# Optimization experiments

Measured on AMD Instinct MI355X. Metric: run time of the kernel, lower is better.

## Reference

```python
import jax, jax.numpy as jnp
import numpy as np

B, N, D, S, H = 64, 4096, 256, 8, 256
ITERS = 3
EPS = 1e-8
SCALE = D ** -0.5


def _ln(x, g, b):
    m = jnp.mean(x, axis=-1, keepdims=True)
    v = jnp.mean((x - m) ** 2, axis=-1, keepdims=True)
    return (x - m) * jax.lax.rsqrt(v + 1e-5) * g + b


def setup_inputs() -> dict:
    key = jax.random.key(0)
    ks = jax.random.split(key, 12)
    s = 0.02
    return {
        'inputs': jax.random.normal(ks[0], (B, N, D), jnp.float32),
        'slot_noise': jax.random.normal(ks[1], (B, S, D), jnp.float32),
        'slots_mean': jax.random.normal(ks[2], (1, 1, D), jnp.float32),
        'slots_logvar': s * jax.random.normal(ks[3], (1, 1, D), jnp.float32),
        'Wq': s * jax.random.normal(ks[4], (D, D), jnp.float32),
        'bq': jnp.zeros((D,), jnp.float32),
        'Wk': s * jax.random.normal(ks[5], (D, D), jnp.float32),
        'bk': jnp.zeros((D,), jnp.float32),
        'Wv': s * jax.random.normal(ks[6], (D, D), jnp.float32),
        'bv': jnp.zeros((D,), jnp.float32),
        'W_ih': s * jax.random.normal(ks[7], (3 * D, D), jnp.float32),
        'b_ih': jnp.zeros((3 * D,), jnp.float32),
        'W_hh': s * jax.random.normal(ks[8], (3 * D, D), jnp.float32),
        'b_hh': jnp.zeros((3 * D,), jnp.float32),
        'W1': s * jax.random.normal(ks[9], (H, D), jnp.float32),
        'b1': jnp.zeros((H,), jnp.float32),
        'W2': s * jax.random.normal(ks[10], (D, H), jnp.float32),
        'b2': jnp.zeros((D,), jnp.float32),
        'g_in': jnp.ones((D,), jnp.float32),
        'bias_in': jnp.zeros((D,), jnp.float32),
        'g_slots': jnp.ones((D,), jnp.float32),
        'bias_slots': jnp.zeros((D,), jnp.float32),
        'g_ff': jnp.ones((D,), jnp.float32),
        'bias_ff': jnp.zeros((D,), jnp.float32),
    }


def reference(inputs, slot_noise, slots_mean, slots_logvar, Wq, bq, Wk, bk, Wv, bv,
              W_ih, b_ih, W_hh, b_hh, W1, b1, W2, b2,
              g_in, bias_in, g_slots, bias_slots, g_ff, bias_ff):
    # slot init: mean + exp(logvar) * noise  (exp(logvar) used as multiplier, as in source)
    slots = slots_mean + jnp.exp(slots_logvar) * slot_noise  # [B,S,D]
    x = _ln(inputs, g_in, bias_in)                            # [B,N,D]
    k = x @ Wk.T + bk
    v = x @ Wv.T + bv
    attn = None
    for _ in range(ITERS):
        slots_prev = slots
        sn = _ln(slots, g_slots, bias_slots)
        q = sn @ Wq.T + bq                                    # [B,S,D]
        dots = jnp.einsum('bid,bjd->bij', q, k) * SCALE       # [B,S,N]
        attn = jax.nn.softmax(dots, axis=1) + EPS             # softmax over slots, no renorm
        updates = jnp.einsum('bjd,bij->bid', v, attn)         # [B,S,D]
        # GRUCell (PyTorch convention)
        gi = updates @ W_ih.T + b_ih                          # [B,S,3D]
        gh = slots_prev @ W_hh.T + b_hh
        i_r, i_z, i_n = jnp.split(gi, 3, axis=-1)
        h_r, h_z, h_n = jnp.split(gh, 3, axis=-1)
        r = jax.nn.sigmoid(i_r + h_r)
        z = jax.nn.sigmoid(i_z + h_z)
        n = jnp.tanh(i_n + r * h_n)
        slots = (1.0 - z) * n + z * slots_prev
        # MLP residual
        sf = _ln(slots, g_ff, bias_ff)
        slots = slots + (jax.nn.relu(sf @ W1.T + b1) @ W2.T + b2)
    return (slots, attn)
```

## Files before the change

### kernel.cpp

```cpp
#include <hip/hip_runtime.h>

typedef unsigned short u16;
typedef __bf16 bf16x8 __attribute__((ext_vector_type(8)));
typedef float f32x4 __attribute__((ext_vector_type(4)));

#define DEV static __device__ __forceinline__

DEV u16 f2bf(float f) {
    unsigned int u = __builtin_bit_cast(unsigned int, f);
    u += 0x7FFFu + ((u >> 16) & 1u);
    return (u16)(u >> 16);
}

DEV bf16x8 frag_ld(const u16* p) {
    return __builtin_bit_cast(bf16x8, *(const uint4*)p);
}

DEV float sigm(float x) { return 1.f / (1.f + __expf(-x)); }

DEV int swz(int idx, int d) { return idx ^ (((d >> 3) & 3) << 4); }

__global__ void kInit(const float* __restrict__ noise, const float* __restrict__ mean,
                      const float* __restrict__ logv, float* __restrict__ slots) {
    int id = blockIdx.x * 256 + threadIdx.x;
    int d = id & 255;
    slots[id] = mean[d] + __expf(logv[d]) * noise[id];
}

__global__ void kT(const float* __restrict__ in, float* __restrict__ out, int R, int C) {
    __shared__ float tile[32][33];
    const int tx = threadIdx.x & 31, ty = threadIdx.x >> 5;
    const int c0 = blockIdx.x * 32, r0 = blockIdx.y * 32;
    #pragma unroll
    for (int i = 0; i < 4; ++i)
        tile[ty + i * 8][tx] = in[(size_t)(r0 + ty + i * 8) * C + c0 + tx];
    __syncthreads();
    #pragma unroll
    for (int i = 0; i < 4; ++i)
        out[(size_t)(c0 + ty + i * 8) * R + r0 + tx] = tile[tx][ty + i * 8];
}

__global__ void kWqk(const float* __restrict__ Wq, const float* __restrict__ Wk,
                     const float* __restrict__ bq, const float* __restrict__ bk,
                     float* __restrict__ Wqk, float* __restrict__ wbc) {
    const int a = blockIdx.x, e = threadIdx.x;
    if (a < 256) {
        float acc = 0.f;
        for (int d = 0; d < 256; ++d) acc += Wq[(size_t)d * 256 + a] * Wk[(size_t)d * 256 + e];
        Wqk[(size_t)a * 256 + e] = acc;
    } else if (a == 256) {
        float acc = 0.f;
        for (int d = 0; d < 256; ++d) acc += bq[d] * Wk[(size_t)d * 256 + e];
        wbc[e] = acc;
    } else {
        float acc = 0.f;
        for (int d = 0; d < 256; ++d) acc += Wq[(size_t)d * 256 + e] * bk[d];
        wbc[256 + e] = acc;
        if (e == 0) {
            float c0 = 0.f;
            for (int d = 0; d < 256; ++d) c0 += bq[d] * bk[d];
            wbc[512] = c0;
        }
    }
}

__global__ __launch_bounds__(256) void kLN(
    const float* __restrict__ X, const float* __restrict__ g, const float* __restrict__ bb,
    u16* __restrict__ XN)
{
    const int w = threadIdx.x >> 6, lane = threadIdx.x & 63;
    const int c = lane << 2;
    const float4 g4 = *(const float4*)(g + c);
    const float4 b4 = *(const float4*)(bb + c);
    const size_t r0 = (size_t)blockIdx.x * 128 + (size_t)w * 32;
    #pragma unroll 4
    for (int i = 0; i < 32; ++i) {
        const float4 x = *(const float4*)(X + (r0 + i) * 256 + c);
        float s1 = x.x + x.y + x.z + x.w;
        float s2 = x.x * x.x + x.y * x.y + x.z * x.z + x.w * x.w;
        #pragma unroll
        for (int o = 32; o > 0; o >>= 1) { s1 += __shfl_xor(s1, o); s2 += __shfl_xor(s2, o); }
        const float mu = s1 * (1.f / 256.f);
        const float rs = rsqrtf(s2 * (1.f / 256.f) - mu * mu + 1e-5f);
        ushort4 pk;
        pk.x = f2bf((x.x - mu) * rs * g4.x + b4.x);
        pk.y = f2bf((x.y - mu) * rs * g4.y + b4.y);
        pk.z = f2bf((x.z - mu) * rs * g4.z + b4.z);
        pk.w = f2bf((x.w - mu) * rs * g4.w + b4.w);
        *(ushort4*)(XN + (r0 + i) * 256 + c) = pk;
    }
}

__global__ __launch_bounds__(256) void kSn(
    const float* __restrict__ slots, const float* __restrict__ gs, const float* __restrict__ bs,
    const float* __restrict__ Wqk, const float* __restrict__ wbc,
    u16* __restrict__ qo, float* __restrict__ qc)
{
    __shared__ float SN[8][256];
    __shared__ float red2[4][8][64];
    const int t = threadIdx.x;
    const int b = blockIdx.y, seg = blockIdx.x;
    const int w = t >> 6, lane = t & 63;
    #pragma unroll
    for (int rr = 0; rr < 2; ++rr) {
        const int r = w * 2 + rr;
        const int c = lane * 4;
        const float4 x = *(const float4*)(slots + ((size_t)b * 8 + r) * 256 + c);
        float s1 = x.x + x.y + x.z + x.w;
        float s2 = x.x * x.x + x.y * x.y + x.z * x.z + x.w * x.w;
        #pragma unroll
        for (int o = 32; o > 0; o >>= 1) { s1 += __shfl_xor(s1, o); s2 += __shfl_xor(s2, o); }
        const float mu = s1 * (1.f / 256.f);
        const float rs = rsqrtf(s2 * (1.f / 256.f) - mu * mu + 1e-5f);
        const float4 g4 = *(const float4*)(gs + c);
        const float4 b4 = *(const float4*)(bs + c);
        SN[r][c + 0] = (x.x - mu) * rs * g4.x + b4.x;
        SN[r][c + 1] = (x.y - mu) * rs * g4.y + b4.y;
        SN[r][c + 2] = (x.z - mu) * rs * g4.z + b4.z;
        SN[r][c + 3] = (x.w - mu) * rs * g4.w + b4.w;
    }
    __syncthreads();
    const int c = seg * 64 + (t & 63);
    const int p = t >> 6;
    float acc[8] = {};
    #pragma unroll 4
    for (int d = p * 64; d < p * 64 + 64; ++d) {
        const float wq = Wqk[(size_t)d * 256 + c];
        #pragma unroll
        for (int r = 0; r < 8; ++r) acc[r] += wq * SN[r][d];
    }
    #pragma unroll
    for (int r = 0; r < 8; ++r) red2[p][r][t & 63] = acc[r];
    __syncthreads();
    const float bb = wbc[c];
    #pragma unroll
    for (int rr = t >> 6; rr < 8; rr += 4) {
        const float s = red2[0][rr][t & 63] + red2[1][rr][t & 63]
                      + red2[2][rr][t & 63] + red2[3][rr][t & 63];
        qo[((size_t)b * 16 + rr) * 256 + c] = f2bf((s + bb) * 0.0625f);
    }
    if (seg == 0) {
        const int r = t >> 5, l = t & 31;
        float a = 0.f;
        #pragma unroll
        for (int d8 = 0; d8 < 8; ++d8) a += SN[r][l * 8 + d8] * wbc[256 + l * 8 + d8];
        #pragma unroll
        for (int o = 16; o > 0; o >>= 1) a += __shfl_xor(a, o);
        if (l == 0) qc[(size_t)b * 8 + r] = 0.0625f * (a + wbc[512]);
    }
}

__global__ __launch_bounds__(256, 2) void kF(
    const u16* __restrict__ Q,
    const float* __restrict__ qcg,
    const u16* __restrict__ XN,
    float* __restrict__ attn_out,
    float* __restrict__ part,
    float* __restrict__ part2,
    int write_attn)
{
    __shared__ __align__(16) u16 T2[256 * 136];
    __shared__ __align__(16) u16 att[16 * 136];
    __shared__ float sred[4][2][4][16];
    const int tid = threadIdx.x;
    const int w = tid >> 6, lane = tid & 63;
    const int quad = lane >> 4, l16 = lane & 15;
    const int b = blockIdx.y, nt = blockIdx.x;
    const int j0 = nt << 9;

    const u16* qb = Q + (size_t)b * 16 * 256;
    bf16x8 qfrag[8];
    #pragma unroll
    for (int k0 = 0; k0 < 8; ++k0)
        qfrag[k0] = frag_ld(qb + l16 * 256 + k0 * 32 + quad * 8);

    float c8[8];
    #pragma unroll
    for (int i = 0; i < 8; ++i) c8[i] = qcg[(size_t)b * 8 + i];

    for (int idx = tid; idx < 8 * 136; idx += 256) att[8 * 136 + idx] = 0;

    f32x4 us[4] = {};
    float sacc[4] = {};

    const u16* xb = XN + ((size_t)b * 4096 + j0) * 256;
    const int qb1 = (quad & 1) << 2;

    for (int st = 0; st < 4; ++st) {
        __syncthreads();
        f32x4 dacc[2] = {};
        #pragma unroll
        for (int n2 = 0; n2 < 2; ++n2) {
            const int jsl = w * 32 + n2 * 16 + l16;
            const u16* xrow = xb + ((size_t)(st * 128 + jsl)) * 256;
            #pragma unroll
            for (int k0 = 0; k0 < 8; ++k0) {
                const uint4 raw = *(const uint4*)(xrow + k0 * 32 + quad * 8);
                dacc[n2] = __builtin_amdgcn_mfma_f32_16x16x32_bf16(
                    qfrag[k0], __builtin_bit_cast(bf16x8, raw), dacc[n2], 0, 0, 0);
                const u16* h = (const u16*)&raw;
                const int dbase = k0 * 32 + quad * 8;
                #pragma unroll
                for (int e = 0; e < 8; ++e)
                    T2[swz((dbase + e) * 136 + jsl, dbase + e)] = h[e];
            }
        }
        #pragma unroll
        for (int n2 = 0; n2 < 2; ++n2) {
            const int jsl = w * 32 + n2 * 16 + l16;
            float v[8];
            #pragma unroll
            for (int r = 0; r < 4; ++r) {
                v[qb1 + r]       = dacc[n2][r];
                v[(qb1 ^ 4) + r] = __shfl_xor(dacc[n2][r], 16);
            }
            #pragma unroll
            for (int i = 0; i < 8; ++i) v[i] += c8[i];
            float m = v[0];
            #pragma unroll
            for (int i = 1; i < 8; ++i) m = fmaxf(m, v[i]);
            float s = 0.f;
            #pragma unroll
            for (int i = 0; i < 8; ++i) { v[i] = __expf(v[i] - m); s += v[i]; }
            const float inv = 1.f / s;
            if (quad < 2) {
                #pragma unroll
                for (int r = 0; r < 4; ++r) {
                    const float a = v[qb1 + r] * inv + 1e-8f;
                    att[(qb1 + r) * 136 + jsl] = f2bf(a);
                    sacc[r] += a;
                    if (write_attn)
                        attn_out[((size_t)b * 8 + qb1 + r) * 4096 + j0 + st * 128 + jsl] = a;
                }
            }
        }
        __syncthreads();
        bf16x8 afrag[4];
        #pragma unroll
        for (int k0 = 0; k0 < 4; ++k0)
            afrag[k0] = frag_ld(att + l16 * 136 + k0 * 32 + quad * 8);
        #pragma unroll
        for (int n2 = 0; n2 < 4; ++n2) {
            const int d = w * 64 + n2 * 16 + l16;
            #pragma unroll
            for (int k0 = 0; k0 < 4; ++k0) {
                const bf16x8 bfr = frag_ld(T2 + swz(d * 136 + k0 * 32 + quad * 8, d));
                us[n2] = __builtin_amdgcn_mfma_f32_16x16x32_bf16(afrag[k0], bfr, us[n2], 0, 0, 0);
            }
        }
    }

    if (quad < 2) {
        #pragma unroll
        for (int r = 0; r < 4; ++r) sred[w][quad][r][l16] = sacc[r];
        #pragma unroll
        for (int n2 = 0; n2 < 4; ++n2)
            #pragma unroll
            for (int r = 0; r < 4; ++r)
                part[(((size_t)nt * 64 + b) * 8 + (quad * 4 + r)) * 256 + w * 64 + n2 * 16 + l16]
                    = us[n2][r];
    }
    __syncthreads();
    if (tid < 8) {
        const int q = tid >> 2, r = tid & 3;
        float s = 0.f;
        #pragma unroll
        for (int ww = 0; ww < 4; ++ww)
            #pragma unroll
            for (int l = 0; l < 16; ++l) s += sred[ww][q][r][l];
        part2[((size_t)nt * 64 + b) * 8 + tid] = s;
    }
}

__global__ __launch_bounds__(256) void kB3(
    const float* __restrict__ part, const float* __restrict__ part2,
    const float* __restrict__ WvT, const float* __restrict__ bv,
    const float* __restrict__ sl_in,
    const float* __restrict__ WihT, const float* __restrict__ bih,
    const float* __restrict__ WhhT, const float* __restrict__ bhh,
    const float* __restrict__ W1T, const float* __restrict__ b1,
    const float* __restrict__ W2T, const float* __restrict__ b2,
    const float* __restrict__ gf, const float* __restrict__ bff,
    float* __restrict__ sl_out)
{
    __shared__ float Ul[2][256], Sl[2][256];
    __shared__ float red[2][4][6][256];
    __shared__ float SNl[2][256];
    __shared__ float cw[2][2][4];
    __shared__ float Ssl[2];
    const int t = threadIdx.x;
    const int kp = t >> 6, c = t & 63;
    const int row0 = blockIdx.x * 2;

    #pragma unroll
    for (int r = 0; r < 2; ++r) {
        const int row = row0 + r;
        const int b = row >> 3, s = row & 7;
        float u = 0.f;
        #pragma unroll
        for (int nt = 0; nt < 8; ++nt)
            u += part[(((size_t)nt * 64 + b) * 8 + s) * 256 + t];
        Ul[r][t] = u;
        Sl[r][t] = sl_in[(size_t)row * 256 + t];
    }
    if (t < 2) {
        const int row = row0 + t;
        const int b = row >> 3, s = row & 7;
        float ss = 0.f;
        #pragma unroll
        for (int nt = 0; nt < 8; ++nt) ss += part2[((size_t)nt * 64 + b) * 8 + s];
        Ssl[t] = ss;
    }
    __syncthreads();

    {
        float va[2][4] = {};
        #pragma unroll 4
        for (int dd = 0; dd < 64; ++dd) {
            const int d = kp * 64 + dd;
            const float* wr = WvT + (size_t)d * 256;
            const float u0 = Ul[0][d], u1 = Ul[1][d];
            #pragma unroll
            for (int cg = 0; cg < 4; ++cg) {
                const float wv = wr[cg * 64 + c];
                va[0][cg] += wv * u0;
                va[1][cg] += wv * u1;
            }
        }
        #pragma unroll
        for (int r = 0; r < 2; ++r)
            #pragma unroll
            for (int cg = 0; cg < 4; ++cg)
                red[r][kp][0][cg * 64 + c] = va[r][cg];
    }
    __syncthreads();
    const float bvt = bv[t];
    float upd2[2];
    #pragma unroll
    for (int r = 0; r < 2; ++r)
        upd2[r] = red[r][0][0][t] + red[r][1][0][t] + red[r][2][0][t] + red[r][3][0][t]
                + Ssl[r] * bvt;
    __syncthreads();
    #pragma unroll
    for (int r = 0; r < 2; ++r) Ul[r][t] = upd2[r];
    __syncthreads();

    float ga[2][4][6] = {};
    #pragma unroll 2
    for (int dd = 0; dd < 64; ++dd) {
        const int d = kp * 64 + dd;
        const float* wi = WihT + (size_t)d * 768;
        const float* wh = WhhT + (size_t)d * 768;
        const float u0 = Ul[0][d], u1 = Ul[1][d];
        const float s0 = Sl[0][d], s1 = Sl[1][d];
        #pragma unroll
        for (int cg = 0; cg < 4; ++cg) {
            const int t2 = cg * 64 + c;
            const float wa = wi[t2], wb = wi[256 + t2], wc = wi[512 + t2];
            const float wd = wh[t2], we = wh[256 + t2], wf = wh[512 + t2];
            ga[0][cg][0] += wa * u0; ga[0][cg][1] += wb * u0; ga[0][cg][2] += wc * u0;
            ga[0][cg][3] += wd * s0; ga[0][cg][4] += we * s0; ga[0][cg][5] += wf * s0;
            ga[1][cg][0] += wa * u1; ga[1][cg][1] += wb * u1; ga[1][cg][2] += wc * u1;
            ga[1][cg][3] += wd * s1; ga[1][cg][4] += we * s1; ga[1][cg][5] += wf * s1;
        }
    }
    #pragma unroll
    for (int r = 0; r < 2; ++r)
        #pragma unroll
        for (int cg = 0; cg < 4; ++cg)
            #pragma unroll
            for (int g = 0; g < 6; ++g)
                red[r][kp][g][cg * 64 + c] = ga[r][cg][g];
    __syncthreads();

    const float b_ir = bih[t], b_iz = bih[256 + t], b_in = bih[512 + t];
    const float b_hr = bhh[t], b_hz = bhh[256 + t], b_hn = bhh[512 + t];
    float hnew[2];
    #pragma unroll
    for (int r = 0; r < 2; ++r) {
        float s6[6];
        #pragma unroll
        for (int g = 0; g < 6; ++g)
            s6[g] = red[r][0][g][t] + red[r][1][g][t] + red[r][2][g][t] + red[r][3][g][t];
        const float rg = sigm(s6[0] + b_ir + s6[3] + b_hr);
        const float zg = sigm(s6[1] + b_iz + s6[4] + b_hz);
        const float ng = tanhf(s6[2] + b_in + rg * (s6[5] + b_hn));
        hnew[r] = (1.f - zg) * ng + zg * Sl[r][t];
    }
    #pragma unroll
    for (int r = 0; r < 2; ++r) {
        float s1 = hnew[r], s2 = hnew[r] * hnew[r];
        #pragma unroll
        for (int o = 32; o > 0; o >>= 1) { s1 += __shfl_xor(s1, o); s2 += __shfl_xor(s2, o); }
        if (c == 0) { cw[r][0][kp] = s1; cw[r][1][kp] = s2; }
    }
    __syncthreads();
    const float gft = gf[t], bfft = bff[t];
    #pragma unroll
    for (int r = 0; r < 2; ++r) {
        const float s1 = cw[r][0][0] + cw[r][0][1] + cw[r][0][2] + cw[r][0][3];
        const float s2 = cw[r][1][0] + cw[r][1][1] + cw[r][1][2] + cw[r][1][3];
        const float mu = s1 * (1.f / 256.f);
        const float rs = rsqrtf(s2 * (1.f / 256.f) - mu * mu + 1e-5f);
        SNl[r][t] = (hnew[r] - mu) * rs * gft + bfft;
    }
    __syncthreads();

    {
        float m1[2][4] = {};
        #pragma unroll 4
        for (int dd = 0; dd < 64; ++dd) {
            const int d = kp * 64 + dd;
            const float* wr = W1T + (size_t)d * 256;
            const float n0 = SNl[0][d], n1 = SNl[1][d];
            #pragma unroll
            for (int cg = 0; cg < 4; ++cg) {
                const float wv = wr[cg * 64 + c];
                m1[0][cg] += wv * n0;
                m1[1][cg] += wv * n1;
            }
        }
        #pragma unroll
        for (int r = 0; r < 2; ++r)
            #pragma unroll
            for (int cg = 0; cg < 4; ++cg)
                red[r][kp][0][cg * 64 + c] = m1[r][cg];
    }
    __syncthreads();
    const float b1t = b1[t];
    float h1v[2];
    #pragma unroll
    for (int r = 0; r < 2; ++r)
        h1v[r] = fmaxf(red[r][0][0][t] + red[r][1][0][t] + red[r][2][0][t] + red[r][3][0][t]
                       + b1t, 0.f);
    __syncthreads();
    #pragma unroll
    for (int r = 0; r < 2; ++r) SNl[r][t] = h1v[r];
    __syncthreads();
    {
        float m2[2][4] = {};
        #pragma unroll 4
        for (int dd = 0; dd < 64; ++dd) {
            const int d = kp * 64 + dd;
            const float* wr = W2T + (size_t)d * 256;
            const float x0 = SNl[0][d], x1 = SNl[1][d];
            #pragma unroll
            for (int cg = 0; cg < 4; ++cg) {
                const float wv = wr[cg * 64 + c];
                m2[0][cg] += wv * x0;
                m2[1][cg] += wv * x1;
            }
        }
        #pragma unroll
        for (int r = 0; r < 2; ++r)
            #pragma unroll
            for (int cg = 0; cg < 4; ++cg)
                red[r][kp][1][cg * 64 + c] = m2[r][cg];
    }
    __syncthreads();
    const float b2t = b2[t];
    #pragma unroll
    for (int r = 0; r < 2; ++r) {
        const float o = red[r][0][1][t] + red[r][1][1][t] + red[r][2][1][t] + red[r][3][1][t];
        sl_out[(size_t)(row0 + r) * 256 + t] = hnew[r] + o + b2t;
    }
}

extern "C" void kernel_launch(void* const* d_in, const int* in_sizes, int n_in,
                              void* d_out, int out_size, void* d_ws, size_t ws_size,
                              hipStream_t stream) {
    const float* inputs = (const float*)d_in[0];
    const float* noise  = (const float*)d_in[1];
    const float* smean  = (const float*)d_in[2];
    const float* slogv  = (const float*)d_in[3];
    const float* Wq  = (const float*)d_in[4];
    const float* bq  = (const float*)d_in[5];
    const float* Wk  = (const float*)d_in[6];
    const float* bk  = (const float*)d_in[7];
    const float* Wv  = (const float*)d_in[8];
    const float* bv  = (const float*)d_in[9];
    const float* Wih = (const float*)d_in[10];
    const float* bih = (const float*)d_in[11];
    const float* Whh = (const float*)d_in[12];
    const float* bhh = (const float*)d_in[13];
    const float* W1  = (const float*)d_in[14];
    const float* b1  = (const float*)d_in[15];
    const float* W2  = (const float*)d_in[16];
    const float* b2  = (const float*)d_in[17];
    const float* gin = (const float*)d_in[18];
    const float* bin = (const float*)d_in[19];
    const float* gs  = (const float*)d_in[20];
    const float* bs  = (const float*)d_in[21];
    const float* gf  = (const float*)d_in[22];
    const float* bff = (const float*)d_in[23];

    char* ws = (char*)d_ws;
    u16*  XNw    = (u16*)(ws);
    u16*  qw     = (u16*)(ws + 134217728ull);
    float* slots = (float*)(ws + 134742016ull);
    float* Wqkw  = (float*)(ws + 135790592ull);
    float* wbc   = (float*)(ws + 136052736ull);
    float* qcw   = (float*)(ws + 136056832ull);
    float* WvT   = (float*)(ws + 136060928ull);
    float* WihT  = (float*)(ws + 136323072ull);
    float* WhhT  = (float*)(ws + 137109504ull);
    float* W1T   = (float*)(ws + 137895936ull);
    float* W2T   = (float*)(ws + 138158080ull);
    float* partw = (float*)(ws + 138420224ull);
    float* part2w= (float*)(ws + 142614528ull);

    float* out = (float*)d_out;
    float* attn_out = out + 131072;

    kInit<<<512, 256, 0, stream>>>(noise, smean, slogv, slots);
    kWqk<<<258, 256, 0, stream>>>(Wq, Wk, bq, bk, Wqkw, wbc);
    kT<<<dim3(8, 8),  256, 0, stream>>>(Wv,  WvT,  256, 256);
    kT<<<dim3(8, 24), 256, 0, stream>>>(Wih, WihT, 768, 256);
    kT<<<dim3(8, 24), 256, 0, stream>>>(Whh, WhhT, 768, 256);
    kT<<<dim3(8, 8),  256, 0, stream>>>(W1,  W1T,  256, 256);
    kT<<<dim3(8, 8),  256, 0, stream>>>(W2,  W2T,  256, 256);
    kLN<<<2048, 256, 0, stream>>>(inputs, gin, bin, XNw);
    for (int it = 0; it < 3; ++it) {
        kSn<<<dim3(4, 64), 256, 0, stream>>>(slots, gs, bs, Wqkw, wbc, qw, qcw);
        kF<<<dim3(8, 64), 256, 0, stream>>>(qw, qcw, XNw, attn_out, partw, part2w, it == 2);
        kB3<<<256, 256, 0, stream>>>(partw, part2w, WvT, bv, slots,
                                     WihT, bih, WhhT, bhh, W1T, b1, W2T, b2, gf, bff,
                                     (it == 2) ? out : slots);
    }
}
```

Measured before the change: 718.3 us.

## Replace LDS-transposed MFMA attn@X with per-wave FP32 FMA accumulation

The second product (attention times normalized inputs) no longer transposes X into shared memory and runs it through MFMA. Each wave instead re-reads its own X rows from global/L2 and accumulates all 8 slots × 8 dims per lane in FP32 registers with FMAs. Partial sums are combined across half-waves by shuffle and across waves through shared memory before the write-out. This drops the heavy scattered 16-bit LDS stores and two barriers per step. In exchange it re-reads X, does the math on scalar FMA units instead of matrix cores, and keeps 64 accumulators per lane, which raises register pressure.

```diff
diff --git a/kernel.cpp b/kernel.cpp
--- a/kernel.cpp
+++ b/kernel.cpp
@@ -18,7 +18,8 @@
 
 DEV float sigm(float x) { return 1.f / (1.f + __expf(-x)); }
 
-DEV int swz(int idx, int d) { return idx ^ (((d >> 3) & 3) << 4); }
+DEV float blo(unsigned u) { return __builtin_bit_cast(float, u << 16); }
+DEV float bhi(unsigned u) { return __builtin_bit_cast(float, u & 0xffff0000u); }
 
 __global__ void kInit(const float* __restrict__ noise, const float* __restrict__ mean,
                       const float* __restrict__ logv, float* __restrict__ slots) {
@@ -159,12 +160,13 @@
     float* __restrict__ part2,
     int write_attn)
 {
-    __shared__ __align__(16) u16 T2[256 * 136];
-    __shared__ __align__(16) u16 att[16 * 136];
+    __shared__ __align__(16) float att32[128][8];
+    __shared__ float usred[4][8][256];
     __shared__ float sred[4][2][4][16];
     const int tid = threadIdx.x;
     const int w = tid >> 6, lane = tid & 63;
     const int quad = lane >> 4, l16 = lane & 15;
+    const int dsg = lane & 31, jg = lane >> 5;
     const int b = blockIdx.y, nt = blockIdx.x;
     const int j0 = nt << 9;
 
@@ -178,16 +180,17 @@
     #pragma unroll
     for (int i = 0; i < 8; ++i) c8[i] = qcg[(size_t)b * 8 + i];
 
-    for (int idx = tid; idx < 8 * 136; idx += 256) att[8 * 136 + idx] = 0;
-
-    f32x4 us[4] = {};
+    float acc[8][8];
+    #pragma unroll
+    for (int i = 0; i < 8; ++i)
+        #pragma unroll
+        for (int e = 0; e < 8; ++e) acc[i][e] = 0.f;
     float sacc[4] = {};
 
     const u16* xb = XN + ((size_t)b * 4096 + j0) * 256;
     const int qb1 = (quad & 1) << 2;
 
     for (int st = 0; st < 4; ++st) {
-        __syncthreads();
         f32x4 dacc[2] = {};
         #pragma unroll
         for (int n2 = 0; n2 < 2; ++n2) {
@@ -195,14 +198,9 @@
             const u16* xrow = xb + ((size_t)(st * 128 + jsl)) * 256;
             #pragma unroll
             for (int k0 = 0; k0 < 8; ++k0) {
-                const uint4 raw = *(const uint4*)(xrow + k0 * 32 + quad * 8);
+                const bf16x8 bfr = frag_ld(xrow + k0 * 32 + quad * 8);
                 dacc[n2] = __builtin_amdgcn_mfma_f32_16x16x32_bf16(
-                    qfrag[k0], __builtin_bit_cast(bf16x8, raw), dacc[n2], 0, 0, 0);
-                const u16* h = (const u16*)&raw;
-                const int dbase = k0 * 32 + quad * 8;
-                #pragma unroll
-                for (int e = 0; e < 8; ++e)
-                    T2[swz((dbase + e) * 136 + jsl, dbase + e)] = h[e];
+                    qfrag[k0], bfr, dacc[n2], 0, 0, 0);
             }
         }
         #pragma unroll
@@ -224,43 +222,71 @@
             for (int i = 0; i < 8; ++i) { v[i] = __expf(v[i] - m); s += v[i]; }
             const float inv = 1.f / s;
             if (quad < 2) {
-                #pragma unroll
-                for (int r = 0; r < 4; ++r) {
-                    const float a = v[qb1 + r] * inv + 1e-8f;
-                    att[(qb1 + r) * 136 + jsl] = f2bf(a);
-                    sacc[r] += a;
-                    if (write_attn)
-                        attn_out[((size_t)b * 8 + qb1 + r) * 4096 + j0 + st * 128 + jsl] = a;
+                float4 av;
+                av.x = v[qb1 + 0] * inv + 1e-8f;
+                av.y = v[qb1 + 1] * inv + 1e-8f;
+                av.z = v[qb1 + 2] * inv + 1e-8f;
+                av.w = v[qb1 + 3] * inv + 1e-8f;
+                sacc[0] += av.x; sacc[1] += av.y; sacc[2] += av.z; sacc[3] += av.w;
+                *(float4*)&att32[jsl][qb1] = av;
+                if (write_attn) {
+                    attn_out[((size_t)b * 8 + qb1 + 0) * 4096 + j0 + st * 128 + jsl] = av.x;
+                    attn_out[((size_t)b * 8 + qb1 + 1) * 4096 + j0 + st * 128 + jsl] = av.y;
+                    attn_out[((size_t)b * 8 + qb1 + 2) * 4096 + j0 + st * 128 + jsl] = av.z;
+                    attn_out[((size_t)b * 8 + qb1 + 3) * 4096 + j0 + st * 128 + jsl] = av.w;
                 }
             }
         }
-        __syncthreads();
-        bf16x8 afrag[4];
-        #pragma unroll
-        for (int k0 = 0; k0 < 4; ++k0)
-            afrag[k0] = frag_ld(att + l16 * 136 + k0 * 32 + quad * 8);
-        #pragma unroll
-        for (int n2 = 0; n2 < 4; ++n2) {
-            const int d = w * 64 + n2 * 16 + l16;
-            #pragma unroll
-            for (int k0 = 0; k0 < 4; ++k0) {
-                const bf16x8 bfr = frag_ld(T2 + swz(d * 136 + k0 * 32 + quad * 8, d));
-                us[n2] = __builtin_amdgcn_mfma_f32_16x16x32_bf16(afrag[k0], bfr, us[n2], 0, 0, 0);
-            }
-        }
-    }
-
+        #pragma unroll 4
+        for (int jj = 0; jj < 16; ++jj) {
+            const int jsl = w * 32 + jj * 2 + jg;
+            const uint4 raw = *(const uint4*)(xb + ((size_t)(st * 128 + jsl)) * 256 + dsg * 8);
+            const float4 a0 = *(const float4*)&att32[jsl][0];
+            const float4 a1 = *(const float4*)&att32[jsl][4];
+            float xf[8];
+            xf[0] = blo(raw.x); xf[1] = bhi(raw.x);
+            xf[2] = blo(raw.y); xf[3] = bhi(raw.y);
+            xf[4] = blo(raw.z); xf[5] = bhi(raw.z);
+            xf[6] = blo(raw.w); xf[7] = bhi(raw.w);
+            #pragma unroll
+            for (int e = 0; e < 8; ++e) {
+                acc[0][e] = fmaf(a0.x, xf[e], acc[0][e]);
+                acc[1][e] = fmaf(a0.y, xf[e], acc[1][e]);
+                acc[2][e] = fmaf(a0.z, xf[e], acc[2][e]);
+                acc[3][e] = fmaf(a0.w, xf[e], acc[3][e]);
+                acc[4][e] = fmaf(a1.x, xf[e], acc[4][e]);
+                acc[5][e] = fmaf(a1.y, xf[e], acc[5][e]);
+                acc[6][e] = fmaf(a1.z, xf[e], acc[6][e]);
+                acc[7][e] = fmaf(a1.w, xf[e], acc[7][e]);
+            }
+        }
+    }
+
+    #pragma unroll
+    for (int i = 0; i < 8; ++i)
+        #pragma unroll
+        for (int e = 0; e < 8; ++e) acc[i][e] += __shfl_xor(acc[i][e], 32);
+    if (jg == 0) {
+        #pragma unroll
+        for (int i = 0; i < 8; ++i) {
+            float4 lo, hi;
+            lo.x = acc[i][0]; lo.y = acc[i][1]; lo.z = acc[i][2]; lo.w = acc[i][3];
+            hi.x = acc[i][4]; hi.y = acc[i][5]; hi.z = acc[i][6]; hi.w = acc[i][7];
+            *(float4*)&usred[w][i][dsg * 8]     = lo;
+            *(float4*)&usred[w][i][dsg * 8 + 4] = hi;
+        }
+    }
     if (quad < 2) {
         #pragma unroll
         for (int r = 0; r < 4; ++r) sred[w][quad][r][l16] = sacc[r];
-        #pragma unroll
-        for (int n2 = 0; n2 < 4; ++n2)
-            #pragma unroll
-            for (int r = 0; r < 4; ++r)
-                part[(((size_t)nt * 64 + b) * 8 + (quad * 4 + r)) * 256 + w * 64 + n2 * 16 + l16]
-                    = us[n2][r];
-    }
-    __syncthreads();
+    }
+    __syncthreads();
+    #pragma unroll
+    for (int i = 0; i < 8; ++i) {
+        const float s = usred[0][i][tid] + usred[1][i][tid]
+                      + usred[2][i][tid] + usred[3][i][tid];
+        part[(((size_t)nt * 64 + b) * 8 + i) * 256 + tid] = s;
+    }
     if (tid < 8) {
         const int q = tid >> 2, r = tid & 3;
         float s = 0.f;
```

After: 733.5 us. 2.1% more time.

## Split fused attention kernel into dots/softmax and update kernels with pre-transposed XN

Applied to the files above, without the earlier changes.

Replaces the fused kF kernel, which transposed the normalized inputs through a large LDS tile every iteration, with a one-time bf16 transpose of XN into a feature-major copy plus two kernels. kD computes dots and the softmax and writes bf16 attention to global memory, and kU computes the updates by MFMA against the transposed XN. Both use finer 128-token tiles, so there are 32 partials instead of 8, and kB3 now sums more partials. It also merges the setup kernels into one launch. The aim is to drop the heavy LDS scatter and raise occupancy, at the cost of an extra 128MB transpose and additional global traffic each iteration.

```diff
diff --git a/kernel.cpp b/kernel.cpp
--- a/kernel.cpp
+++ b/kernel.cpp
@@ -18,50 +18,65 @@
 
 DEV float sigm(float x) { return 1.f / (1.f + __expf(-x)); }
 
-DEV int swz(int idx, int d) { return idx ^ (((d >> 3) & 3) << 4); }
-
-__global__ void kInit(const float* __restrict__ noise, const float* __restrict__ mean,
-                      const float* __restrict__ logv, float* __restrict__ slots) {
-    int id = blockIdx.x * 256 + threadIdx.x;
-    int d = id & 255;
-    slots[id] = mean[d] + __expf(logv[d]) * noise[id];
-}
-
-__global__ void kT(const float* __restrict__ in, float* __restrict__ out, int R, int C) {
+__global__ __launch_bounds__(256) void kSetup(
+    const float* __restrict__ noise, const float* __restrict__ mean,
+    const float* __restrict__ logv, float* __restrict__ slots,
+    const float* __restrict__ Wq, const float* __restrict__ Wk,
+    const float* __restrict__ bq, const float* __restrict__ bk,
+    float* __restrict__ Wqk, float* __restrict__ wbc,
+    const float* __restrict__ Wv,  float* __restrict__ WvT,
+    const float* __restrict__ Wih, float* __restrict__ WihT,
+    const float* __restrict__ Whh, float* __restrict__ WhhT,
+    const float* __restrict__ W1,  float* __restrict__ W1T,
+    const float* __restrict__ W2,  float* __restrict__ W2T)
+{
     __shared__ float tile[32][33];
-    const int tx = threadIdx.x & 31, ty = threadIdx.x >> 5;
-    const int c0 = blockIdx.x * 32, r0 = blockIdx.y * 32;
+    const int bid = blockIdx.x, t = threadIdx.x;
+    if (bid < 512) {
+        const int id = bid * 256 + t;
+        const int d = id & 255;
+        slots[id] = mean[d] + __expf(logv[d]) * noise[id];
+        return;
+    }
+    if (bid < 770) {
+        const int a = bid - 512, e = t;
+        if (a < 256) {
+            float acc = 0.f;
+            for (int d = 0; d < 256; ++d) acc += Wq[(size_t)d * 256 + a] * Wk[(size_t)d * 256 + e];
+            Wqk[(size_t)a * 256 + e] = acc;
+        } else if (a == 256) {
+            float acc = 0.f;
+            for (int d = 0; d < 256; ++d) acc += bq[d] * Wk[(size_t)d * 256 + e];
+            wbc[e] = acc;
+        } else {
+            float acc = 0.f;
+            for (int d = 0; d < 256; ++d) acc += Wq[(size_t)d * 256 + e] * bk[d];
+            wbc[256 + e] = acc;
+            if (e == 0) {
+                float c0 = 0.f;
+                for (int d = 0; d < 256; ++d) c0 += bq[d] * bk[d];
+                wbc[512] = c0;
+            }
+        }
+        return;
+    }
+    const int rb = bid - 770;
+    const float* in; float* outp; int R, k;
+    if (rb < 64)       { in = Wv;  outp = WvT;  R = 256; k = rb; }
+    else if (rb < 256) { in = Wih; outp = WihT; R = 768; k = rb - 64; }
+    else if (rb < 448) { in = Whh; outp = WhhT; R = 768; k = rb - 256; }
+    else if (rb < 512) { in = W1;  outp = W1T;  R = 256; k = rb - 448; }
+    else               { in = W2;  outp = W2T;  R = 256; k = rb - 512; }
+    const int bx = k & 7, by = k >> 3;
+    const int tx = t & 31, ty = t >> 5;
+    const int c0 = bx * 32, r0 = by * 32;
     #pragma unroll
     for (int i = 0; i < 4; ++i)
-        tile[ty + i * 8][tx] = in[(size_t)(r0 + ty + i * 8) * C + c0 + tx];
+        tile[ty + i * 8][tx] = in[(size_t)(r0 + ty + i * 8) * 256 + c0 + tx];
     __syncthreads();
     #pragma unroll
     for (int i = 0; i < 4; ++i)
-        out[(size_t)(c0 + ty + i * 8) * R + r0 + tx] = tile[tx][ty + i * 8];
-}
-
-__global__ void kWqk(const float* __restrict__ Wq, const float* __restrict__ Wk,
-                     const float* __restrict__ bq, const float* __restrict__ bk,
-                     float* __restrict__ Wqk, float* __restrict__ wbc) {
-    const int a = blockIdx.x, e = threadIdx.x;
-    if (a < 256) {
-        float acc = 0.f;
-        for (int d = 0; d < 256; ++d) acc += Wq[(size_t)d * 256 + a] * Wk[(size_t)d * 256 + e];
-        Wqk[(size_t)a * 256 + e] = acc;
-    } else if (a == 256) {
-        float acc = 0.f;
-        for (int d = 0; d < 256; ++d) acc += bq[d] * Wk[(size_t)d * 256 + e];
-        wbc[e] = acc;
-    } else {
-        float acc = 0.f;
-        for (int d = 0; d < 256; ++d) acc += Wq[(size_t)d * 256 + e] * bk[d];
-        wbc[256 + e] = acc;
-        if (e == 0) {
-            float c0 = 0.f;
-            for (int d = 0; d < 256; ++d) c0 += bq[d] * bk[d];
-            wbc[512] = c0;
-        }
-    }
+        outp[(size_t)(c0 + ty + i * 8) * R + r0 + tx] = tile[tx][ty + i * 8];
 }
 
 __global__ __launch_bounds__(256) void kLN(
@@ -91,6 +106,34 @@
     }
 }
 
+__global__ __launch_bounds__(256) void kT16(
+    const u16* __restrict__ XN, u16* __restrict__ XNT)
+{
+    __shared__ ushort2 S[64][33];
+    const int t = threadIdx.x;
+    const int jt = blockIdx.x, dt = blockIdx.y, b = blockIdx.z;
+    const int j0 = jt << 6, d0 = dt << 6;
+    const u16* in = XN + (size_t)b * 4096 * 256;
+    u16* outp = XNT + (size_t)b * 256 * 4096;
+    const int tx = t & 31, ty = t >> 5;
+    #pragma unroll
+    for (int i = 0; i < 8; ++i) {
+        const int j = ty + i * 8;
+        S[j][tx] = *(const ushort2*)(in + (size_t)(j0 + j) * 256 + d0 + tx * 2);
+    }
+    __syncthreads();
+    const int tx2 = t & 31, ty2 = t >> 5;
+    #pragma unroll
+    for (int i = 0; i < 8; ++i) {
+        const int d = ty2 + i * 8;
+        const ushort2 a = S[tx2 * 2 + 0][d >> 1];
+        const ushort2 bq2 = S[tx2 * 2 + 1][d >> 1];
+        ushort2 v;
+        if (ty2 & 1) { v.x = a.y; v.y = bq2.y; } else { v.x = a.x; v.y = bq2.x; }
+        *(ushort2*)(outp + (size_t)(d0 + d) * 4096 + j0 + tx2 * 2) = v;
+    }
+}
+
 __global__ __launch_bounds__(256) void kSn(
     const float* __restrict__ slots, const float* __restrict__ gs, const float* __restrict__ bs,
     const float* __restrict__ Wqk, const float* __restrict__ wbc,
@@ -150,125 +193,127 @@
     }
 }
 
-__global__ __launch_bounds__(256, 2) void kF(
+__global__ __launch_bounds__(256) void kD(
     const u16* __restrict__ Q,
     const float* __restrict__ qcg,
     const u16* __restrict__ XN,
+    u16* __restrict__ att,
     float* __restrict__ attn_out,
-    float* __restrict__ part,
     float* __restrict__ part2,
     int write_attn)
 {
-    __shared__ __align__(16) u16 T2[256 * 136];
-    __shared__ __align__(16) u16 att[16 * 136];
-    __shared__ float sred[4][2][4][16];
+    __shared__ float sred[4][2][4];
     const int tid = threadIdx.x;
     const int w = tid >> 6, lane = tid & 63;
     const int quad = lane >> 4, l16 = lane & 15;
-    const int b = blockIdx.y, nt = blockIdx.x;
-    const int j0 = nt << 9;
-
-    const u16* qb = Q + (size_t)b * 16 * 256;
+    const int qb1 = (quad & 1) << 2;
+    const int b = blockIdx.y, js = blockIdx.x;
+    const int j0 = js << 7;
+
+    const u16* qptr = Q + (size_t)b * 16 * 256;
     bf16x8 qfrag[8];
     #pragma unroll
     for (int k0 = 0; k0 < 8; ++k0)
-        qfrag[k0] = frag_ld(qb + l16 * 256 + k0 * 32 + quad * 8);
+        qfrag[k0] = frag_ld(qptr + l16 * 256 + k0 * 32 + quad * 8);
 
     float c8[8];
     #pragma unroll
     for (int i = 0; i < 8; ++i) c8[i] = qcg[(size_t)b * 8 + i];
 
-    for (int idx = tid; idx < 8 * 136; idx += 256) att[8 * 136 + idx] = 0;
-
-    f32x4 us[4] = {};
     float sacc[4] = {};
-
     const u16* xb = XN + ((size_t)b * 4096 + j0) * 256;
-    const int qb1 = (quad & 1) << 2;
-
-    for (int st = 0; st < 4; ++st) {
-        __syncthreads();
-        f32x4 dacc[2] = {};
-        #pragma unroll
-        for (int n2 = 0; n2 < 2; ++n2) {
-            const int jsl = w * 32 + n2 * 16 + l16;
-            const u16* xrow = xb + ((size_t)(st * 128 + jsl)) * 256;
-            #pragma unroll
-            for (int k0 = 0; k0 < 8; ++k0) {
-                const uint4 raw = *(const uint4*)(xrow + k0 * 32 + quad * 8);
-                dacc[n2] = __builtin_amdgcn_mfma_f32_16x16x32_bf16(
-                    qfrag[k0], __builtin_bit_cast(bf16x8, raw), dacc[n2], 0, 0, 0);
-                const u16* h = (const u16*)&raw;
-                const int dbase = k0 * 32 + quad * 8;
-                #pragma unroll
-                for (int e = 0; e < 8; ++e)
-                    T2[swz((dbase + e) * 136 + jsl, dbase + e)] = h[e];
+
+    f32x4 dacc[2] = {};
+    #pragma unroll
+    for (int n2 = 0; n2 < 2; ++n2) {
+        const int jsl = w * 32 + n2 * 16 + l16;
+        const u16* xrow = xb + (size_t)jsl * 256;
+        #pragma unroll
+        for (int k0 = 0; k0 < 8; ++k0) {
+            const bf16x8 bfr = frag_ld(xrow + k0 * 32 + quad * 8);
+            dacc[n2] = __builtin_amdgcn_mfma_f32_16x16x32_bf16(qfrag[k0], bfr, dacc[n2], 0, 0, 0);
+        }
+    }
+    #pragma unroll
+    for (int n2 = 0; n2 < 2; ++n2) {
+        const int jsl = w * 32 + n2 * 16 + l16;
+        float v[8];
+        #pragma unroll
+        for (int r = 0; r < 4; ++r) {
+            v[qb1 + r]       = dacc[n2][r];
+            v[(qb1 ^ 4) + r] = __shfl_xor(dacc[n2][r], 16);
+        }
+        #pragma unroll
+        for (int i = 0; i < 8; ++i) v[i] += c8[i];
+        float m = v[0];
+        #pragma unroll
+        for (int i = 1; i < 8; ++i) m = fmaxf(m, v[i]);
+        float s = 0.f;
+        #pragma unroll
+        for (int i = 0; i < 8; ++i) { v[i] = __expf(v[i] - m); s += v[i]; }
+        const float inv = 1.f / s;
+        if (quad < 2) {
+            #pragma unroll
+            for (int r = 0; r < 4; ++r) {
+                const float a = v[qb1 + r] * inv + 1e-8f;
+                sacc[r] += a;
+                att[((size_t)b * 16 + qb1 + r) * 4096 + j0 + jsl] = f2bf(a);
+                if (write_attn)
+                    attn_out[((size_t)b * 8 + qb1 + r) * 4096 + j0 + jsl] = a;
             }
         }
-        #pragma unroll
-        for (int n2 = 0; n2 < 2; ++n2) {
-            const int jsl = w * 32 + n2 * 16 + l16;
-            float v[8];
-            #pragma unroll
-            for (int r = 0; r < 4; ++r) {
-                v[qb1 + r]       = dacc[n2][r];
-                v[(qb1 ^ 4) + r] = __shfl_xor(dacc[n2][r], 16);
-            }
-            #pragma unroll
-            for (int i = 0; i < 8; ++i) v[i] += c8[i];
-            float m = v[0];
-            #pragma unroll
-            for (int i = 1; i < 8; ++i) m = fmaxf(m, v[i]);
-            float s = 0.f;
-            #pragma unroll
-            for (int i = 0; i < 8; ++i) { v[i] = __expf(v[i] - m); s += v[i]; }
-            const float inv = 1.f / s;
-            if (quad < 2) {
-                #pragma unroll
-                for (int r = 0; r < 4; ++r) {
-                    const float a = v[qb1 + r] * inv + 1e-8f;
-                    att[(qb1 + r) * 136 + jsl] = f2bf(a);
-                    sacc[r] += a;
-                    if (write_attn)
-                        attn_out[((size_t)b * 8 + qb1 + r) * 4096 + j0 + st * 128 + jsl] = a;
-                }
-            }
-        }
-        __syncthreads();
-        bf16x8 afrag[4];
-        #pragma unroll
-        for (int k0 = 0; k0 < 4; ++k0)
-            afrag[k0] = frag_ld(att + l16 * 136 + k0 * 32 + quad * 8);
-        #pragma unroll
-        for (int n2 = 0; n2 < 4; ++n2) {
-            const int d = w * 64 + n2 * 16 + l16;
-            #pragma unroll
-            for (int k0 = 0; k0 < 4; ++k0) {
-                const bf16x8 bfr = frag_ld(T2 + swz(d * 136 + k0 * 32 + quad * 8, d));
-                us[n2] = __builtin_amdgcn_mfma_f32_16x16x32_bf16(afrag[k0], bfr, us[n2], 0, 0, 0);
-            }
-        }
-    }
-
-    if (quad < 2) {
-        #pragma unroll
-        for (int r = 0; r < 4; ++r) sred[w][quad][r][l16] = sacc[r];
-        #pragma unroll
-        for (int n2 = 0; n2 < 4; ++n2)
-            #pragma unroll
-            for (int r = 0; r < 4; ++r)
-                part[(((size_t)nt * 64 + b) * 8 + (quad * 4 + r)) * 256 + w * 64 + n2 * 16 + l16]
-                    = us[n2][r];
+    }
+    #pragma unroll
+    for (int r = 0; r < 4; ++r)
+        #pragma unroll
+        for (int o = 1; o < 16; o <<= 1) sacc[r] += __shfl_xor(sacc[r], o);
+    if (l16 == 0 && quad < 2) {
+        #pragma unroll
+        for (int r = 0; r < 4; ++r) sred[w][quad][r] = sacc[r];
     }
     __syncthreads();
     if (tid < 8) {
         const int q = tid >> 2, r = tid & 3;
-        float s = 0.f;
-        #pragma unroll
-        for (int ww = 0; ww < 4; ++ww)
-            #pragma unroll
-            for (int l = 0; l < 16; ++l) s += sred[ww][q][r][l];
-        part2[((size_t)nt * 64 + b) * 8 + tid] = s;
+        const float s = sred[0][q][r] + sred[1][q][r] + sred[2][q][r] + sred[3][q][r];
+        part2[((size_t)js * 64 + b) * 8 + tid] = s;
+    }
+}
+
+__global__ __launch_bounds__(256) void kU(
+    const u16* __restrict__ att,
+    const u16* __restrict__ XNT,
+    float* __restrict__ part)
+{
+    const int tid = threadIdx.x;
+    const int w = tid >> 6, lane = tid & 63;
+    const int quad = lane >> 4, l16 = lane & 15;
+    const int b = blockIdx.y, js = blockIdx.x;
+    const int j0 = js << 7;
+
+    const u16* ab = att + ((size_t)b * 16 + l16) * 4096 + j0;
+    bf16x8 afrag[4];
+    #pragma unroll
+    for (int ks = 0; ks < 4; ++ks)
+        afrag[ks] = frag_ld(ab + ks * 32 + quad * 8);
+
+    f32x4 acc[4] = {};
+    const u16* xtb = XNT + (size_t)b * 256 * 4096 + j0;
+    #pragma unroll
+    for (int dt = 0; dt < 4; ++dt) {
+        const u16* xrow = xtb + (size_t)(w * 64 + dt * 16 + l16) * 4096;
+        #pragma unroll
+        for (int ks = 0; ks < 4; ++ks) {
+            const bf16x8 bfr = frag_ld(xrow + ks * 32 + quad * 8);
+            acc[dt] = __builtin_amdgcn_mfma_f32_16x16x32_bf16(afrag[ks], bfr, acc[dt], 0, 0, 0);
+        }
+    }
+    if (quad < 2) {
+        const size_t pb = ((size_t)js * 64 + b) * 8;
+        #pragma unroll
+        for (int dt = 0; dt < 4; ++dt)
+            #pragma unroll
+            for (int r = 0; r < 4; ++r)
+                part[(pb + quad * 4 + r) * 256 + w * 64 + dt * 16 + l16] = acc[dt][r];
     }
 }
 
@@ -296,11 +341,13 @@
     for (int r = 0; r < 2; ++r) {
         const int row = row0 + r;
         const int b = row >> 3, s = row & 7;
-        float u = 0.f;
-        #pragma unroll
-        for (int nt = 0; nt < 8; ++nt)
-            u += part[(((size_t)nt * 64 + b) * 8 + s) * 256 + t];
-        Ul[r][t] = u;
+        float ua0 = 0.f, ua1 = 0.f;
+        #pragma unroll 8
+        for (int u = 0; u < 32; u += 2) {
+            ua0 += part[(((size_t)u * 64 + b) * 8 + s) * 256 + t];
+            ua1 += part[(((size_t)(u + 1) * 64 + b) * 8 + s) * 256 + t];
+        }
+        Ul[r][t] = ua0 + ua1;
         Sl[r][t] = sl_in[(size_t)row * 256 + t];
     }
     if (t < 2) {
@@ -308,7 +355,7 @@
         const int b = row >> 3, s = row & 7;
         float ss = 0.f;
         #pragma unroll
-        for (int nt = 0; nt < 8; ++nt) ss += part2[((size_t)nt * 64 + b) * 8 + s];
+        for (int u = 0; u < 32; ++u) ss += part2[((size_t)u * 64 + b) * 8 + s];
         Ssl[t] = ss;
     }
     __syncthreads();
@@ -496,33 +543,33 @@
 
     char* ws = (char*)d_ws;
     u16*  XNw    = (u16*)(ws);
-    u16*  qw     = (u16*)(ws + 134217728ull);
-    float* slots = (float*)(ws + 134742016ull);
-    float* Wqkw  = (float*)(ws + 135790592ull);
-    float* wbc   = (float*)(ws + 136052736ull);
-    float* qcw   = (float*)(ws + 136056832ull);
-    float* WvT   = (float*)(ws + 136060928ull);
-    float* WihT  = (float*)(ws + 136323072ull);
-    float* WhhT  = (float*)(ws + 137109504ull);
-    float* W1T   = (float*)(ws + 137895936ull);
-    float* W2T   = (float*)(ws + 138158080ull);
-    float* partw = (float*)(ws + 138420224ull);
-    float* part2w= (float*)(ws + 142614528ull);
+    u16*  XNTw   = (u16*)(ws + 134217728ull);
+    u16*  qw     = (u16*)(ws + 268435456ull);
+    float* slots = (float*)(ws + 268959744ull);
+    float* Wqkw  = (float*)(ws + 269484032ull);
+    float* wbc   = (float*)(ws + 269746176ull);
+    float* qcw   = (float*)(ws + 269750272ull);
+    float* WvT   = (float*)(ws + 269754368ull);
+    float* WihT  = (float*)(ws + 270016512ull);
+    float* WhhT  = (float*)(ws + 270802944ull);
+    float* W1T   = (float*)(ws + 271589376ull);
+    float* W2T   = (float*)(ws + 271851520ull);
+    u16*  attb   = (u16*)(ws + 272113664ull);
+    float* partw = (float*)(ws + 280502272ull);
+    float* part2w= (float*)(ws + 297279488ull);
 
     float* out = (float*)d_out;
     float* attn_out = out + 131072;
 
-    kInit<<<512, 256, 0, stream>>>(noise, smean, slogv, slots);
-    kWqk<<<258, 256, 0, stream>>>(Wq, Wk, bq, bk, Wqkw, wbc);
-    kT<<<dim3(8, 8),  256, 0, stream>>>(Wv,  WvT,  256, 256);
-    kT<<<dim3(8, 24), 256, 0, stream>>>(Wih, WihT, 768, 256);
-    kT<<<dim3(8, 24), 256, 0, stream>>>(Whh, WhhT, 768, 256);
-    kT<<<dim3(8, 8),  256, 0, stream>>>(W1,  W1T,  256, 256);
-    kT<<<dim3(8, 8),  256, 0, stream>>>(W2,  W2T,  256, 256);
+    kSetup<<<1346, 256, 0, stream>>>(noise, smean, slogv, slots,
+                                     Wq, Wk, bq, bk, Wqkw, wbc,
+                                     Wv, WvT, Wih, WihT, Whh, WhhT, W1, W1T, W2, W2T);
     kLN<<<2048, 256, 0, stream>>>(inputs, gin, bin, XNw);
+    kT16<<<dim3(64, 4, 64), 256, 0, stream>>>(XNw, XNTw);
     for (int it = 0; it < 3; ++it) {
         kSn<<<dim3(4, 64), 256, 0, stream>>>(slots, gs, bs, Wqkw, wbc, qw, qcw);
-        kF<<<dim3(8, 64), 256, 0, stream>>>(qw, qcw, XNw, attn_out, partw, part2w, it == 2);
+        kD<<<dim3(32, 64), 256, 0, stream>>>(qw, qcw, XNw, attb, attn_out, part2w, it == 2);
+        kU<<<dim3(32, 64), 256, 0, stream>>>(attb, XNTw, partw);
         kB3<<<256, 256, 0, stream>>>(partw, part2w, WvT, bv, slots,
                                      WihT, bih, WhhT, bhh, W1T, b1, W2T, b2, gf, bff,
                                      (it == 2) ? out : slots);
```

Result: slower. 863.9 us (+20.3%).
